# Kernel tuning notes

Hardware: AMD Instinct MI355X
Metric: run time of the kernel (lower is better)

Reference implementation:

```python
import jax, jax.numpy as jnp
import numpy as np

NUM_HEADS = 16
HEAD_DIM = 128
D = NUM_HEADS * HEAD_DIM  # 2048
B, S = 4, 2048
NEG = jnp.finfo(jnp.float32).min


def setup_inputs() -> dict:
    key = jax.random.key(0)
    ks = jax.random.split(key, 6)
    scale = 1.0 / np.sqrt(D)
    return {
        "hidden_states": jax.random.normal(ks[0], (B, S, D), jnp.float32),
        "wq": jax.random.normal(ks[1], (D, D), jnp.float32) * scale,
        "wk": jax.random.normal(ks[2], (D, D), jnp.float32) * scale,
        "wv": jax.random.normal(ks[3], (D, D), jnp.float32) * scale,
        "wo": jax.random.normal(ks[4], (D, D), jnp.float32) * scale,
        "bo": jnp.zeros((D,), jnp.float32),
    }


def _split_heads(x):
    b, s, _ = x.shape
    return x.reshape(b, s, NUM_HEADS, HEAD_DIM).transpose(0, 2, 1, 3)  # [B,H,S,Dh]


def reference(hidden_states, wq, wk, wv, wo, bo):
    # projections (nn.Linear: x @ W^T), no bias for q/k/v
    q = _split_heads(hidden_states @ wq.T).astype(jnp.float32)
    k = _split_heads(hidden_states @ wk.T).astype(jnp.float32)
    v = _split_heads(hidden_states @ wv.T)
    # GPT-Neo: NO 1/sqrt(d) scaling
    scores = jnp.einsum("bhqd,bhkd->bhqk", q, k)  # [B,H,S,S] fp32
    s = scores.shape[-1]
    causal = jnp.tril(jnp.ones((s, s), bool))  # [S,S]
    scores = jnp.where(causal[None, None], scores, NEG)
    attn_weights = jax.nn.softmax(scores, axis=-1).astype(v.dtype)
    # dropout is identity at eval (p=0.0)
    attn_output = jnp.einsum("bhqk,bhkd->bhqd", attn_weights, v)
    attn_output = attn_output.transpose(0, 2, 1, 3).reshape(hidden_states.shape)
    attn_output = attn_output @ wo.T + bo
    return attn_output, attn_weights
```

## Files before the change

kernel.cpp:

```cpp
#include <hip/hip_runtime.h>

#define DEVFN static __device__ __forceinline__

typedef _Float16 f16;
typedef f16 f16x8 __attribute__((ext_vector_type(8)));
typedef f16 f16x4 __attribute__((ext_vector_type(4)));
typedef float f32x4 __attribute__((ext_vector_type(4)));
typedef short short8 __attribute__((ext_vector_type(8)));

constexpr int Bc = 4, Hn = 16, Sn = 2048, DH = 128, Dn = 2048;
constexpr long MROWS = (long)Bc * Sn;
constexpr long LDQK = 2 * Dn;

template <typename T, typename C>
DEVFN auto mfma_impl(T a, T b, C c, int)
    -> decltype(__builtin_amdgcn_mfma_f32_16x16x32_f16(a, b, c, 0, 0, 0)) {
  return __builtin_amdgcn_mfma_f32_16x16x32_f16(a, b, c, 0, 0, 0);
}
template <typename T, typename C>
DEVFN C mfma_impl(T a, T b, C c, long) {
  return __builtin_amdgcn_mfma_f32_16x16x32_f16(
      __builtin_bit_cast(short8, a), __builtin_bit_cast(short8, b), c, 0, 0, 0);
}
DEVFN f32x4 MFMA(f16x8 a, f16x8 b, f32x4 c) { return mfma_impl(a, b, c, 0); }

DEVFN void nt_store(float* p, float v) { __builtin_nontemporal_store(v, p); }
DEVFN void nt_store4(float* p, f32x4 v) {
  __builtin_nontemporal_store(v, (f32x4*)p);
}

DEVFN void gld_lds16(const f16* g, f16* s) {
  __builtin_amdgcn_global_load_lds(
      (const __attribute__((address_space(1))) unsigned int*)g,
      (__attribute__((address_space(3))) unsigned int*)s, 16, 0, 0);
}

DEVFN void stage_tile(const f16* __restrict__ g, long ld, f16* __restrict__ s) {
  const int t = threadIdx.x;
  const int rr = t >> 3;
  const int cb = (t & 7) * 16;
#pragma unroll
  for (int ch = 0; ch < 4; ++ch) {
    const int r = ch * 32 + rr;
    const int scb = cb ^ ((r & 7) << 4);
    gld_lds16(g + (long)r * ld + (scb >> 1), s + r * 64 + (cb >> 1));
  }
}

DEVFN void stage_tile128(const f16* __restrict__ g, long ld, f16* __restrict__ s) {
  const int t = threadIdx.x;
  const int rr = t >> 4;
  const int cb = (t & 15) * 16;
#pragma unroll
  for (int ch = 0; ch < 8; ++ch) {
    const int r = ch * 16 + rr;
    const int scb = cb ^ ((r & 7) << 4);
    gld_lds16(g + (long)r * ld + (scb >> 1), s + r * 128 + (cb >> 1));
  }
}

DEVFN f16x8 ldfrag(const f16* s, int row, int kelem) {
  const int cb = (kelem * 2) ^ ((row & 7) << 4);
  return *(const f16x8*)(s + row * 64 + (cb >> 1));
}

DEVFN f16x8 ldfrag128(const f16* s, int row, int kelem) {
  const int cb = (kelem * 2) ^ ((row & 7) << 4);
  return *(const f16x8*)((const char*)s + row * 256 + cb);
}

DEVFN f16x8 ldfrag64(const f16* s, int row, int kelem) {
  const int cb = (kelem * 2) ^ ((row & 7) << 4);
  return *(const f16x8*)((const char*)s + row * 128 + cb);
}

__global__ __launch_bounds__(256) void k_cvt(const float* __restrict__ x,
                                             f16* __restrict__ y, long n) {
  long i = ((long)blockIdx.x * blockDim.x + threadIdx.x) * 4;
  if (i >= n) return;
  float4 v = *(const float4*)(x + i);
  f16x4 h;
  h[0] = (f16)v.x; h[1] = (f16)v.y; h[2] = (f16)v.z; h[3] = (f16)v.w;
  *(f16x4*)(y + i) = h;
}

__global__ __launch_bounds__(256) void k_cvt4(const float* __restrict__ x0,
                                              const float* __restrict__ x1,
                                              const float* __restrict__ x2,
                                              const float* __restrict__ x3,
                                              f16* __restrict__ y0,
                                              f16* __restrict__ y1,
                                              f16* __restrict__ y2,
                                              f16* __restrict__ y3, long n) {
  const float* x = (blockIdx.y == 0) ? x0 : (blockIdx.y == 1) ? x1
                  : (blockIdx.y == 2) ? x2 : x3;
  f16* y = (blockIdx.y == 0) ? y0 : (blockIdx.y == 1) ? y1
          : (blockIdx.y == 2) ? y2 : y3;
  long i = ((long)blockIdx.x * blockDim.x + threadIdx.x) * 4;
  if (i >= n) return;
  float4 v = *(const float4*)(x + i);
  f16x4 h;
  h[0] = (f16)v.x; h[1] = (f16)v.y; h[2] = (f16)v.z; h[3] = (f16)v.w;
  *(f16x4*)(y + i) = h;
}

__global__ __launch_bounds__(256) void k_zfill(float* __restrict__ wts) {
  const int bh = blockIdx.x, qt = blockIdx.y;
  const int ncols = Sn - (qt + 1) * 128;
  if (ncols <= 0) return;
  float* base = wts + (long)bh * Sn * Sn + (long)qt * 128 * Sn + (qt + 1) * 128;
  const int tid = threadIdx.x;
  const f32x4 z = {0.f, 0.f, 0.f, 0.f};
  for (int r = 0; r < 128; ++r) {
    float* rowp = base + (long)r * Sn;
    for (int c = tid * 4; c < ncols; c += 1024) nt_store4(rowp + c, z);
  }
}

template <int OUTMODE>
__global__ __launch_bounds__(256) void k_gemm_bt(
    const f16* __restrict__ A, long ldA, const f16* __restrict__ B, long ldB,
    int K, f16* __restrict__ oh, float* __restrict__ of,
    const float* __restrict__ bias, long ldC) {
  const int nwgx = gridDim.x;
  const int nwg = nwgx * gridDim.y;
  const int bid = blockIdx.y * nwgx + blockIdx.x;
  const int cpx = nwg >> 3;
  const int swz = (bid & 7) * cpx + (bid >> 3);
  const int nt = swz % nwgx, mt = swz / nwgx;
  __shared__ __align__(16) f16 sA[2][128 * 64];
  __shared__ __align__(16) f16 sB[2][128 * 64];
  const int tid = threadIdx.x, w = tid >> 6, lane = tid & 63;
  const int wm = (w >> 1) * 64, wn = (w & 1) * 64;
  const int lr = lane & 15, lg = lane >> 4;
  f32x4 acc[4][4] = {};
  const f16* Ab = A + (long)mt * 128 * ldA;
  const f16* Bb = B + (long)nt * 128 * ldB;

  stage_tile(Ab, ldA, sA[0]);
  stage_tile(Bb, ldB, sB[0]);
  __syncthreads();

  int cur = 0;
  for (int kt = 0; kt < K; kt += 64) {
    if (kt + 64 < K) {
      stage_tile(Ab + kt + 64, ldA, sA[cur ^ 1]);
      stage_tile(Bb + kt + 64, ldB, sB[cur ^ 1]);
    }
#pragma unroll
    for (int kk = 0; kk < 64; kk += 32) {
      f16x8 ahf[4], bhf[4];
#pragma unroll
      for (int m = 0; m < 4; ++m) ahf[m] = ldfrag(sA[cur], wm + m * 16 + lr, kk + lg * 8);
#pragma unroll
      for (int n = 0; n < 4; ++n) bhf[n] = ldfrag(sB[cur], wn + n * 16 + lr, kk + lg * 8);
#pragma unroll
      for (int m = 0; m < 4; ++m)
#pragma unroll
        for (int n = 0; n < 4; ++n) acc[m][n] = MFMA(ahf[m], bhf[n], acc[m][n]);
    }
    __syncthreads();
    cur ^= 1;
  }

#pragma unroll
  for (int m = 0; m < 4; ++m)
#pragma unroll
    for (int n = 0; n < 4; ++n) {
      const int col = nt * 128 + wn + n * 16 + lr;
#pragma unroll
      for (int r = 0; r < 4; ++r) {
        const long row = (long)mt * 128 + wm + m * 16 + lg * 4 + r;
        const float cv = acc[m][n][r];
        const long idx = row * ldC + col;
        if constexpr (OUTMODE == 1) {
          oh[idx] = (f16)cv;
        } else {
          nt_store(of + idx, cv + bias[col]);
        }
      }
    }
}

__global__ __launch_bounds__(256) void k_attn(const f16* __restrict__ qk16,
                                              const f16* __restrict__ vT,
                                              float* __restrict__ wts,
                                              f16* __restrict__ ctx) {
  const int wgid = blockIdx.x;
  const int xcd = wgid & 7, slot = wgid >> 3;
  const int bh = xcd + 8 * (slot >> 4);
  const int qt = 15 - (slot & 15);
  const int b = bh >> 4, h = bh & 15;
  const int tid = threadIdx.x, wv = tid >> 6, lane = tid & 63;
  const int lr = lane & 15, lg = lane >> 4;
  const f16* Qb = qk16 + ((long)b * Sn + qt * 128) * LDQK + h * DH;
  const f16* Kb = qk16 + (long)b * Sn * LDQK + Dn + h * DH;
  const f16* Vb = vT + (long)h * DH * MROWS + (long)b * Sn;
  float* Wrow = wts + (long)bh * Sn * Sn + (long)qt * 128 * Sn;
  __shared__ __align__(16) f16 sK[2][128 * 128];
  __shared__ __align__(16) f16 sQW[128 * 64];

  const int krr = tid >> 4;
  const int kce = (tid & 15) * 8;
  const int kcb = kce * 2;
  f16x8 kpf[8];

#define PRE_K(kt_)                                                              \
  {                                                                             \
    const long kbase = (long)(kt_)*128;                                         \
    _Pragma("unroll") for (int ch = 0; ch < 8; ++ch) kpf[ch] =                  \
        *(const f16x8*)(Kb + (kbase + ch * 16 + krr) * LDQK + kce);             \
  }
#define PUB_K(buf)                                                              \
  {                                                                             \
    _Pragma("unroll") for (int ch = 0; ch < 8; ++ch) {                          \
      const int r = ch * 16 + krr;                                              \
      *(f16x8*)((char*)(buf) + r * 256 + (kcb ^ ((r & 7) << 4))) = kpf[ch];     \
    }                                                                           \
  }

  stage_tile128(Qb, LDQK, sK[0]);
  PRE_K(0);
  __syncthreads();
  const int wq0 = wv * 32;
  f16x8 qf[2][4];
#pragma unroll
  for (int m = 0; m < 2; ++m)
#pragma unroll
    for (int kk = 0; kk < 4; ++kk)
      qf[m][kk] = ldfrag128(sK[0], wq0 + m * 16 + lr, kk * 32 + lg * 8);
  __syncthreads();
  PUB_K(sK[0]);
  if (qt > 0) PRE_K(1);
  __syncthreads();
  int cur = 0;

  float rs[2][4] = {};
  for (int kt = 0; kt <= qt; ++kt) {
    f32x4 acc[2][8] = {};
#pragma unroll
    for (int kk = 0; kk < 4; ++kk) {
      f16x8 bf[8];
#pragma unroll
      for (int n = 0; n < 8; ++n) bf[n] = ldfrag128(sK[cur], n * 16 + lr, kk * 32 + lg * 8);
#pragma unroll
      for (int m = 0; m < 2; ++m)
#pragma unroll
        for (int n = 0; n < 8; ++n) acc[m][n] = MFMA(qf[m][kk], bf[n], acc[m][n]);
    }
    if (kt + 1 <= qt) PUB_K(sK[cur ^ 1]);
    PRE_K(kt + 2 <= qt ? kt + 2 : 0);
    const bool diag = (kt == qt);
#pragma unroll
    for (int m = 0; m < 2; ++m)
#pragma unroll
      for (int r = 0; r < 4; ++r) {
        const int row = wq0 + m * 16 + lg * 4 + r;
        float ts = 0.f;
#pragma unroll
        for (int n = 0; n < 8; ++n) {
          const bool ok = !diag || (n * 16 + lr) <= row;
          ts += ok ? __expf(acc[m][n][r]) : 0.f;
        }
#pragma unroll
        for (int o = 1; o < 16; o <<= 1) ts += __shfl_xor(ts, o, 64);
        rs[m][r] += ts;
      }
    __syncthreads();
    cur ^= 1;
  }
  float ri[2][4];
#pragma unroll
  for (int m = 0; m < 2; ++m)
#pragma unroll
    for (int r = 0; r < 4; ++r) ri[m][r] = 1.f / rs[m][r];

  PUB_K(sK[cur ^ 1]);
  if (qt > 0) PRE_K(1);
  __syncthreads();
  cur ^= 1;

  f32x4 pacc[2][8] = {};
  for (int kt = 0; kt <= qt; ++kt) {
    f32x4 sacc[2][8] = {};
#pragma unroll
    for (int kk = 0; kk < 4; ++kk) {
      f16x8 bf[8];
#pragma unroll
      for (int n = 0; n < 8; ++n) bf[n] = ldfrag128(sK[cur], n * 16 + lr, kk * 32 + lg * 8);
#pragma unroll
      for (int m = 0; m < 2; ++m)
#pragma unroll
        for (int n = 0; n < 8; ++n) sacc[m][n] = MFMA(qf[m][kk], bf[n], sacc[m][n]);
    }
    if (kt + 1 <= qt) PUB_K(sK[cur ^ 1]);
    if (kt + 2 <= qt) PRE_K(kt + 2);
    const bool diag = (kt == qt);
#pragma unroll
    for (int hf = 0; hf < 2; ++hf) {
#pragma unroll
      for (int m = 0; m < 2; ++m)
#pragma unroll
        for (int n = hf * 4; n < hf * 4 + 4; ++n) {
          const int col = n * 16 + lr;
          const int scol = col - hf * 64;
#pragma unroll
          for (int r = 0; r < 4; ++r) {
            const int row = wq0 + m * 16 + lg * 4 + r;
            float w = __expf(sacc[m][n][r]) * ri[m][r];
            if (diag && col > row) w = 0.f;
            nt_store(Wrow + (long)row * Sn + kt * 128 + col, w);
            *(f16*)((char*)sQW + row * 128 + ((scol * 2) ^ ((row & 7) << 4))) = (f16)w;
          }
        }
#pragma unroll
      for (int kk = 0; kk < 2; ++kk) {
        f16x8 af[2], bfr[8];
#pragma unroll
        for (int m = 0; m < 2; ++m)
          af[m] = ldfrag64(sQW, wq0 + m * 16 + lr, kk * 32 + lg * 8);
#pragma unroll
        for (int n = 0; n < 8; ++n)
          bfr[n] = *(const f16x8*)(Vb + (long)(n * 16 + lr) * MROWS + kt * 128 + hf * 64 + kk * 32 + lg * 8);
#pragma unroll
        for (int m = 0; m < 2; ++m)
#pragma unroll
          for (int n = 0; n < 8; ++n) pacc[m][n] = MFMA(af[m], bfr[n], pacc[m][n]);
      }
    }
    __syncthreads();
    cur ^= 1;
  }

#pragma unroll
  for (int m = 0; m < 2; ++m)
#pragma unroll
    for (int n = 0; n < 8; ++n) {
      const int d = n * 16 + lr;
#pragma unroll
      for (int r = 0; r < 4; ++r) {
        const int q = qt * 128 + wq0 + m * 16 + lg * 4 + r;
        ctx[(long)(b * Sn + q) * Dn + h * DH + d] = (f16)pacc[m][n][r];
      }
    }
#undef PRE_K
#undef PUB_K
}

extern "C" void kernel_launch(void* const* d_in, const int* in_sizes, int n_in,
                              void* d_out, int out_size, void* d_ws, size_t ws_size,
                              hipStream_t stream) {
  const float* hid = (const float*)d_in[0];
  const float* wq = (const float*)d_in[1];
  const float* wk = (const float*)d_in[2];
  const float* wv = (const float*)d_in[3];
  const float* wo = (const float*)d_in[4];
  const float* bo = (const float*)d_in[5];
  float* out = (float*)d_out;
  float* wts = out + (long)Bc * Sn * Dn;

  char* ws = (char*)d_ws;
  const long MB = 1 << 20;
  f16* h16 = (f16*)(ws + 0 * MB);
  f16* wqk16 = (f16*)(ws + 32 * MB);
  f16* wv16 = (f16*)(ws + 48 * MB);
  f16* wo16 = (f16*)(ws + 56 * MB);
  f16* qk16 = (f16*)(ws + 64 * MB);
  f16* vT = (f16*)(ws + 128 * MB);
  f16* ctx = (f16*)(ws + 160 * MB);

  const long nH = (long)Bc * Sn * Dn;
  const long nW = (long)Dn * Dn;

  k_cvt<<<nH / 1024, 256, 0, stream>>>(hid, h16, nH);
  k_cvt4<<<dim3(nW / 1024, 4), 256, 0, stream>>>(
      wq, wk, wv, wo, wqk16, wqk16 + nW, wv16, wo16, nW);
  k_zfill<<<dim3(64, 16), 256, 0, stream>>>(wts);

  k_gemm_bt<1><<<dim3(32, 64), 256, 0, stream>>>(
      h16, Dn, wqk16, Dn, Dn, qk16, nullptr, nullptr, LDQK);
  k_gemm_bt<1><<<dim3(64, 16), 256, 0, stream>>>(
      wv16, Dn, h16, Dn, Dn, vT, nullptr, nullptr, MROWS);
  k_attn<<<1024, 256, 0, stream>>>(qk16, vT, wts, ctx);
  k_gemm_bt<2><<<dim3(16, 64), 256, 0, stream>>>(
      ctx, Dn, wo16, Dn, Dn, nullptr, out, bo, Dn);
}
```

Before: 873.3 us.

## Merge conversions into one launch and co-schedule QK/V GEMMs with zero-fill

Replaces the two fp32-to-fp16 conversion kernels with a single launch covering the hidden states and all four weights. The QK and V projection GEMMs and the upper-triangle zero-fill of the attention weights now share one grid, with every fourth block doing zero-fill. The intent is to cut launch gaps and overlap the store-bound zero-fill with the compute-bound GEMMs. The interleaving changes how blocks map to XCDs and caches, and the zero-fill blocks get no work beyond index 1024 because they return early.

```diff
diff --git a/kernel.cpp b/kernel.cpp
--- a/kernel.cpp
+++ b/kernel.cpp
@@ -74,54 +74,125 @@
   return *(const f16x8*)((const char*)s + row * 128 + cb);
 }
 
-__global__ __launch_bounds__(256) void k_cvt(const float* __restrict__ x,
-                                             f16* __restrict__ y, long n) {
-  long i = ((long)blockIdx.x * blockDim.x + threadIdx.x) * 4;
-  if (i >= n) return;
+__global__ __launch_bounds__(256) void k_cvt_all(
+    const float* __restrict__ hid, const float* __restrict__ wq,
+    const float* __restrict__ wk, const float* __restrict__ wv,
+    const float* __restrict__ wo, f16* __restrict__ h16,
+    f16* __restrict__ wqk16, f16* __restrict__ wv16, f16* __restrict__ wo16) {
+  const int y = blockIdx.y;
+  const long nW = (long)Dn * Dn;
+  const float* x;
+  f16* out;
+  if (y < 4) {
+    x = hid + (long)y * nW;
+    out = h16 + (long)y * nW;
+  } else if (y == 4) {
+    x = wq; out = wqk16;
+  } else if (y == 5) {
+    x = wk; out = wqk16 + nW;
+  } else if (y == 6) {
+    x = wv; out = wv16;
+  } else {
+    x = wo; out = wo16;
+  }
+  const long i = ((long)blockIdx.x * 256 + threadIdx.x) * 4;
   float4 v = *(const float4*)(x + i);
   f16x4 h;
   h[0] = (f16)v.x; h[1] = (f16)v.y; h[2] = (f16)v.z; h[3] = (f16)v.w;
-  *(f16x4*)(y + i) = h;
-}
-
-__global__ __launch_bounds__(256) void k_cvt4(const float* __restrict__ x0,
-                                              const float* __restrict__ x1,
-                                              const float* __restrict__ x2,
-                                              const float* __restrict__ x3,
-                                              f16* __restrict__ y0,
-                                              f16* __restrict__ y1,
-                                              f16* __restrict__ y2,
-                                              f16* __restrict__ y3, long n) {
-  const float* x = (blockIdx.y == 0) ? x0 : (blockIdx.y == 1) ? x1
-                  : (blockIdx.y == 2) ? x2 : x3;
-  f16* y = (blockIdx.y == 0) ? y0 : (blockIdx.y == 1) ? y1
-          : (blockIdx.y == 2) ? y2 : y3;
-  long i = ((long)blockIdx.x * blockDim.x + threadIdx.x) * 4;
-  if (i >= n) return;
-  float4 v = *(const float4*)(x + i);
-  f16x4 h;
-  h[0] = (f16)v.x; h[1] = (f16)v.y; h[2] = (f16)v.z; h[3] = (f16)v.w;
-  *(f16x4*)(y + i) = h;
-}
-
-__global__ __launch_bounds__(256) void k_zfill(float* __restrict__ wts) {
-  const int bh = blockIdx.x, qt = blockIdx.y;
-  const int ncols = Sn - (qt + 1) * 128;
-  if (ncols <= 0) return;
-  float* base = wts + (long)bh * Sn * Sn + (long)qt * 128 * Sn + (qt + 1) * 128;
-  const int tid = threadIdx.x;
-  const f32x4 z = {0.f, 0.f, 0.f, 0.f};
-  for (int r = 0; r < 128; ++r) {
-    float* rowp = base + (long)r * Sn;
-    for (int c = tid * 4; c < ncols; c += 1024) nt_store4(rowp + c, z);
-  }
-}
-
-template <int OUTMODE>
-__global__ __launch_bounds__(256) void k_gemm_bt(
-    const f16* __restrict__ A, long ldA, const f16* __restrict__ B, long ldB,
-    int K, f16* __restrict__ oh, float* __restrict__ of,
-    const float* __restrict__ bias, long ldC) {
+  *(f16x4*)(out + i) = h;
+}
+
+DEVFN void gemm_body(const f16* __restrict__ A, long ldA,
+                     const f16* __restrict__ B, long ldB, int K,
+                     f16* __restrict__ oh, long ldC, int nt, int mt,
+                     f16* sA, f16* sB) {
+  const int tid = threadIdx.x, w = tid >> 6, lane = tid & 63;
+  const int wm = (w >> 1) * 64, wn = (w & 1) * 64;
+  const int lr = lane & 15, lg = lane >> 4;
+  f32x4 acc[4][4] = {};
+  const f16* Ab = A + (long)mt * 128 * ldA;
+  const f16* Bb = B + (long)nt * 128 * ldB;
+
+  stage_tile(Ab, ldA, sA);
+  stage_tile(Bb, ldB, sB);
+  __syncthreads();
+
+  int cur = 0;
+  for (int kt = 0; kt < K; kt += 64) {
+    if (kt + 64 < K) {
+      stage_tile(Ab + kt + 64, ldA, sA + (cur ^ 1) * (128 * 64));
+      stage_tile(Bb + kt + 64, ldB, sB + (cur ^ 1) * (128 * 64));
+    }
+    const f16* cA = sA + cur * (128 * 64);
+    const f16* cB = sB + cur * (128 * 64);
+#pragma unroll
+    for (int kk = 0; kk < 64; kk += 32) {
+      f16x8 ahf[4], bhf[4];
+#pragma unroll
+      for (int m = 0; m < 4; ++m) ahf[m] = ldfrag(cA, wm + m * 16 + lr, kk + lg * 8);
+#pragma unroll
+      for (int n = 0; n < 4; ++n) bhf[n] = ldfrag(cB, wn + n * 16 + lr, kk + lg * 8);
+#pragma unroll
+      for (int m = 0; m < 4; ++m)
+#pragma unroll
+        for (int n = 0; n < 4; ++n) acc[m][n] = MFMA(ahf[m], bhf[n], acc[m][n]);
+    }
+    __syncthreads();
+    cur ^= 1;
+  }
+
+#pragma unroll
+  for (int m = 0; m < 4; ++m)
+#pragma unroll
+    for (int n = 0; n < 4; ++n) {
+      const int col = nt * 128 + wn + n * 16 + lr;
+#pragma unroll
+      for (int r = 0; r < 4; ++r) {
+        const long row = (long)mt * 128 + wm + m * 16 + lg * 4 + r;
+        oh[row * ldC + col] = (f16)acc[m][n][r];
+      }
+    }
+}
+
+__global__ __launch_bounds__(256) void k_fused(
+    const f16* __restrict__ h16, const f16* __restrict__ wqk16,
+    const f16* __restrict__ wv16, f16* __restrict__ qk16, f16* __restrict__ vT,
+    float* __restrict__ wts) {
+  __shared__ __align__(16) f16 sA[2 * 128 * 64];
+  __shared__ __align__(16) f16 sB[2 * 128 * 64];
+  const int bid = blockIdx.x;
+  if ((bid & 3) == 3) {
+    const int zid = bid >> 2;
+    const int bh = zid & 63, qt = zid >> 6;
+    const int ncols = Sn - (qt + 1) * 128;
+    if (ncols <= 0) return;
+    float* base = wts + (long)bh * Sn * Sn + (long)qt * 128 * Sn + (qt + 1) * 128;
+    const int tid = threadIdx.x;
+    const f32x4 z = {0.f, 0.f, 0.f, 0.f};
+    for (int r = 0; r < 128; ++r) {
+      float* rowp = base + (long)r * Sn;
+      for (int c = tid * 4; c < ncols; c += 1024) nt_store4(rowp + c, z);
+    }
+    return;
+  }
+  const int gid = 3 * (bid >> 2) + (bid & 3);
+  if (gid < 2048) {
+    const int cpx = 2048 >> 3;
+    const int swz = (gid & 7) * cpx + (gid >> 3);
+    const int nt = swz & 31, mt = swz >> 5;
+    gemm_body(h16, Dn, wqk16, Dn, Dn, qk16, LDQK, nt, mt, sA, sB);
+  } else {
+    const int sb = gid - 2048;
+    const int cpx = 1024 >> 3;
+    const int swz = (sb & 7) * cpx + (sb >> 3);
+    const int nt = swz & 63, mt = swz >> 6;
+    gemm_body(wv16, Dn, h16, Dn, Dn, vT, MROWS, nt, mt, sA, sB);
+  }
+}
+
+__global__ __launch_bounds__(256) void k_gemm_wo(
+    const f16* __restrict__ A, const f16* __restrict__ B,
+    float* __restrict__ of, const float* __restrict__ bias) {
   const int nwgx = gridDim.x;
   const int nwg = nwgx * gridDim.y;
   const int bid = blockIdx.y * nwgx + blockIdx.x;
@@ -134,18 +205,18 @@
   const int wm = (w >> 1) * 64, wn = (w & 1) * 64;
   const int lr = lane & 15, lg = lane >> 4;
   f32x4 acc[4][4] = {};
-  const f16* Ab = A + (long)mt * 128 * ldA;
-  const f16* Bb = B + (long)nt * 128 * ldB;
-
-  stage_tile(Ab, ldA, sA[0]);
-  stage_tile(Bb, ldB, sB[0]);
+  const f16* Ab = A + (long)mt * 128 * Dn;
+  const f16* Bb = B + (long)nt * 128 * Dn;
+
+  stage_tile(Ab, Dn, sA[0]);
+  stage_tile(Bb, Dn, sB[0]);
   __syncthreads();
 
   int cur = 0;
-  for (int kt = 0; kt < K; kt += 64) {
-    if (kt + 64 < K) {
-      stage_tile(Ab + kt + 64, ldA, sA[cur ^ 1]);
-      stage_tile(Bb + kt + 64, ldB, sB[cur ^ 1]);
+  for (int kt = 0; kt < Dn; kt += 64) {
+    if (kt + 64 < Dn) {
+      stage_tile(Ab + kt + 64, Dn, sA[cur ^ 1]);
+      stage_tile(Bb + kt + 64, Dn, sB[cur ^ 1]);
     }
 #pragma unroll
     for (int kk = 0; kk < 64; kk += 32) {
@@ -171,13 +242,7 @@
 #pragma unroll
       for (int r = 0; r < 4; ++r) {
         const long row = (long)mt * 128 + wm + m * 16 + lg * 4 + r;
-        const float cv = acc[m][n][r];
-        const long idx = row * ldC + col;
-        if constexpr (OUTMODE == 1) {
-          oh[idx] = (f16)cv;
-        } else {
-          nt_store(of + idx, cv + bias[col]);
-        }
+        nt_store(of + row * Dn + col, acc[m][n][r] + bias[col]);
       }
     }
 }
@@ -369,19 +434,9 @@
   f16* vT = (f16*)(ws + 128 * MB);
   f16* ctx = (f16*)(ws + 160 * MB);
 
-  const long nH = (long)Bc * Sn * Dn;
-  const long nW = (long)Dn * Dn;
-
-  k_cvt<<<nH / 1024, 256, 0, stream>>>(hid, h16, nH);
-  k_cvt4<<<dim3(nW / 1024, 4), 256, 0, stream>>>(
-      wq, wk, wv, wo, wqk16, wqk16 + nW, wv16, wo16, nW);
-  k_zfill<<<dim3(64, 16), 256, 0, stream>>>(wts);
-
-  k_gemm_bt<1><<<dim3(32, 64), 256, 0, stream>>>(
-      h16, Dn, wqk16, Dn, Dn, qk16, nullptr, nullptr, LDQK);
-  k_gemm_bt<1><<<dim3(64, 16), 256, 0, stream>>>(
-      wv16, Dn, h16, Dn, Dn, vT, nullptr, nullptr, MROWS);
+  k_cvt_all<<<dim3(4096, 8), 256, 0, stream>>>(
+      hid, wq, wk, wv, wo, h16, wqk16, wv16, wo16);
+  k_fused<<<4096, 256, 0, stream>>>(h16, wqk16, wv16, qk16, vT, wts);
   k_attn<<<1024, 256, 0, stream>>>(qk16, vT, wts, ctx);
-  k_gemm_bt<2><<<dim3(16, 64), 256, 0, stream>>>(
-      ctx, Dn, wo16, Dn, Dn, nullptr, out, bo, Dn);
-}
+  k_gemm_wo<<<dim3(16, 64), 256, 0, stream>>>(ctx, wo16, out, bo);
+}
```

New measurement: 815.9 us. 6.6% less time.
